# Performance work log

Hardware: AMD Instinct MI355X
Metric: run time of the kernel (lower is better)

## Reference

```python
import jax, jax.numpy as jnp
import numpy as np
import math

N, E, MUL = 10000, 160000, 128
D = MUL * 4  # 128x0e (128) + 128x1o (384) = 512
NEURONS = 32
EDGE_ATTR_DIM = 32
WEIGHT_NUMEL = 4 * MUL  # 4 uvu tensor-product paths, 128 weights each


def ssp(x):
    return jax.nn.softplus(x) - math.log(2.0)


def irrep_linear(x, W0, b0, W1):
    # o3.Linear on 128x0e+128x1o: mixes mul channels within each irrep, fan-in normalized,
    # bias only on scalar (0e) block.
    s = x[:, :MUL] @ (W0 / jnp.sqrt(MUL)) + b0
    v = x[:, MUL:].reshape(-1, MUL, 3)
    v = jnp.einsum('num,uv->nvm', v, W1) / jnp.sqrt(MUL)
    return jnp.concatenate([s, v.reshape(-1, MUL * 3)], axis=-1)


def inner_product(a, b):
    # InnerProduct: uuu channel-wise irrep inner product, 1/sqrt(dim) normalized
    s = a[:, :MUL] * b[:, :MUL]
    va = a[:, MUL:].reshape(-1, MUL, 3)
    vb = b[:, MUL:].reshape(-1, MUL, 3)
    v = jnp.einsum('num,num->nu', va, vb) / jnp.sqrt(3.0)
    return jnp.concatenate([s, v], axis=-1)


def norm_gate(x, W1, b1, W2, b2):
    # NormGate: per-channel norms of l>0 irreps -> MLP gates -> gate l>0 channels
    v = x[:, MUL:].reshape(-1, MUL, 3)
    norm_v = jnp.sqrt(jnp.sum(v * v, axis=-1) + 1e-12)      # [n, 128]
    f0 = jnp.concatenate([x[:, :MUL], norm_v], axis=-1)     # [n, 256]
    g = jax.nn.silu(f0 @ W1 + b1) @ W2 + b2                 # [n, 256]
    gated = v * g[:, MUL:, None]
    return jnp.concatenate([g[:, :MUL], gated.reshape(-1, MUL * 3)], axis=-1)


def mlp2(x, Wa, Wb):
    # e3nn FullyConnectedNet: fan-in normalized, ssp nonlinearity on hidden layer only
    return ssp(x @ (Wa / jnp.sqrt(Wa.shape[0]))) @ (Wb / jnp.sqrt(Wb.shape[0]))


def setup_inputs():
    key = jax.random.key(0)
    ks = jax.random.split(key, 20)
    r = lambda i, shp: jax.random.normal(ks[i], shp, dtype=jnp.float32)
    return {
        'x': r(0, (N, D)),
        'edge_index': jax.random.randint(ks[1], (2, E), 0, N, dtype=jnp.int32),
        'edge_attr': jax.random.uniform(ks[2], (E, EDGE_ATTR_DIM), dtype=jnp.float32),
        'edge_sh': r(3, (E, 4)),
        'Wp0': r(4, (MUL, MUL)), 'bp0': jnp.zeros((MUL,), jnp.float32), 'Wp1': r(5, (MUL, MUL)),
        'ngW1': r(6, (2 * MUL, 2 * MUL)) / 16.0, 'ngb1': jnp.zeros((2 * MUL,), jnp.float32),
        'ngW2': r(7, (2 * MUL, 2 * MUL)) / 16.0, 'ngb2': jnp.zeros((2 * MUL,), jnp.float32),
        'Wn0': r(8, (MUL, MUL)), 'bn0': jnp.zeros((MUL,), jnp.float32), 'Wn1': r(9, (MUL, MUL)),
        'fcnW1': r(10, (EDGE_ATTR_DIM, NEURONS)), 'fcnW2': r(11, (NEURONS, WEIGHT_NUMEL)),
        'l0W1': r(12, (3 * MUL, NEURONS)), 'l0W2': r(13, (NEURONS, WEIGHT_NUMEL)),
        'Wo0': r(14, (MUL, MUL)), 'bo0': jnp.zeros((MUL,), jnp.float32), 'Wo1': r(15, (MUL, MUL)),
    }


def reference(x, edge_index, edge_attr, edge_sh, Wp0, bp0, Wp1, ngW1, ngb1, ngW2, ngb2,
              Wn0, bn0, Wn1, fcnW1, fcnW2, l0W1, l0W2, Wo0, bo0, Wo1):
    edge_dst, edge_src = edge_index[0], edge_index[1]
    # invariant edge descriptor s0 from pre-linear + inner product
    pre_x = irrep_linear(x, Wp0, bp0, Wp1)
    ip = inner_product(pre_x[edge_dst], pre_x[edge_src])[:, MUL:]             # [E,128]
    s0 = jnp.concatenate([pre_x[edge_dst][:, :MUL], pre_x[edge_src][:, :MUL], ip], axis=-1)  # [E,384]
    # norm-gate + linear on node features
    x = norm_gate(x, ngW1, ngb1, ngW2, ngb2)
    x = irrep_linear(x, Wn0, bn0, Wn1)
    self_x = x
    # per-edge tensor-product weights: fc_node(edge_attr) * layer_l0(s0)
    w = mlp2(edge_attr, fcnW1, fcnW2) * mlp2(s0, l0W1, l0W2)                   # [E,512]
    w1, w2, w3, w4 = w[:, :MUL], w[:, MUL:2 * MUL], w[:, 2 * MUL:3 * MUL], w[:, 3 * MUL:]
    xs = x[edge_src]
    xs0 = xs[:, :MUL]                     # [E,128]
    xs1 = xs[:, MUL:].reshape(E, MUL, 3)  # [E,128,3]
    sh0 = edge_sh[:, 0:1]
    sh1 = edge_sh[:, 1:4]
    # uvu CG tensor product paths: 0ex0e->0e, 0ex1o->1o, 1ox0e->1o, 1ox1o->0e
    c0, c1 = 0.5, jnp.sqrt(3.0) / 2.0  # path norm sqrt(ir_out.dim / n_paths)
    out0 = c0 * (w1 * xs0 * sh0 + w4 * jnp.einsum('eum,em->eu', xs1, sh1) / jnp.sqrt(3.0))
    out1 = c1 * (w2[:, :, None] * xs0[:, :, None] * sh1[:, None, :]
                 + w3[:, :, None] * xs1 * sh0[:, :, None])
    edge_feat = jnp.concatenate([out0, out1.reshape(E, MUL * 3)], axis=-1)     # [E,512]
    # scatter-aggregate to destination nodes, residual, output linear
    out = jax.ops.segment_sum(edge_feat, edge_dst, num_segments=N)
    out = out + self_x
    return irrep_linear(out, Wo0, bo0, Wo1)
```

## Files before the change

kernel.cpp:

```cpp
#include <hip/hip_runtime.h>
#include <hip/hip_fp16.h>
#include <math.h>

#define NN 10000
#define EE 160000

#define RS128 0.08838834764831845f
#define RS384 0.05103103630798287f
#define RS32  0.17677669529663687f
#define R3    0.57735026918962576f
#define C1V   0.86602540378443865f

typedef _Float16 half8 __attribute__((ext_vector_type(8)));
typedef float f32x4 __attribute__((ext_vector_type(4)));

__device__ __forceinline__ float sspf(float x) {
    return fmaxf(x, 0.0f) + log1pf(__expf(-fabsf(x))) - 0.69314718055994530942f;
}

__global__ __launch_bounds__(256) void k_pack(
    const float* __restrict__ W, _Float16* __restrict__ P, int K, int N) {
    int idx = blockIdx.x * 256 + threadIdx.x;
    if (idx >= K * N) return;
    const int KS = K >> 5;
    int j = idx & 7, lane = (idx >> 3) & 63, rest = idx >> 9;
    int ks = rest % KS, ct = rest / KS;
    int k = ks * 32 + ((lane >> 4) << 3) + j;
    int c = ct * 16 + (lane & 15);
    P[idx] = (_Float16)W[k * N + c];
}

__global__ __launch_bounds__(256) void k_irrep_m(
    const float* __restrict__ X, const _Float16* __restrict__ pW0,
    const float* __restrict__ b0, const _Float16* __restrict__ pW1,
    float* __restrict__ out) {
    __shared__ _Float16 Xr[4][16][136];
    const int t = threadIdx.x, lane = t & 63, w = t >> 6;
    const int nb = blockIdx.x * 16;
    for (int idx = t; idx < 16 * 128; idx += 256) {
        int n = idx >> 7, c4 = idx & 127;
        const float4 v = *(const float4*)(X + (size_t)(nb + n) * 512 + 4 * c4);
        float vals[4] = {v.x, v.y, v.z, v.w};
        int c = 4 * c4;
#pragma unroll
        for (int j = 0; j < 4; ++j) {
            int cc = c + j;
            if (cc < 128) Xr[0][n][cc] = (_Float16)vals[j];
            else { int d = cc - 128; Xr[1 + d % 3][n][d / 3] = (_Float16)vals[j]; }
        }
    }
    __syncthreads();
    const _Float16* pW = (w == 0) ? pW0 : pW1;
    const int row16 = lane & 15, kg = lane >> 4;
    f32x4 acc[8];
    const f32x4 zero = {0.0f, 0.0f, 0.0f, 0.0f};
#pragma unroll
    for (int ct = 0; ct < 8; ++ct) acc[ct] = zero;
    for (int ks = 0; ks < 4; ++ks) {
        const half8 a = *(const half8*)&Xr[w][row16][ks * 32 + kg * 8];
#pragma unroll
        for (int ct = 0; ct < 8; ++ct) {
            const half8 b = *(const half8*)(pW + (((ct * 4 + ks) * 64 + lane) << 3));
            acc[ct] = __builtin_amdgcn_mfma_f32_16x16x32_f16(a, b, acc[ct], 0, 0, 0);
        }
    }
#pragma unroll
    for (int ct = 0; ct < 8; ++ct) {
        const int col = ct * 16 + row16;
        const float bb = (w == 0) ? b0[col] : 0.0f;
#pragma unroll
        for (int r = 0; r < 4; ++r) {
            const int node = nb + kg * 4 + r;
            const float val = acc[ct][r] * RS128 + bb;
            if (w == 0) out[(size_t)node * 512 + col] = val;
            else out[(size_t)node * 512 + 128 + 3 * col + (w - 1)] = val;
        }
    }
}

__global__ __launch_bounds__(256) void k_self_m(
    const float* __restrict__ X,
    const _Float16* __restrict__ png1, const float* __restrict__ ngb1,
    const _Float16* __restrict__ png2, const float* __restrict__ ngb2,
    const _Float16* __restrict__ pWn0, const float* __restrict__ bn0,
    const _Float16* __restrict__ pWn1,
    float* __restrict__ selfx) {
    __shared__ _Float16 f0h[16][264];
    __shared__ _Float16 t1h[16][264];
    __shared__ _Float16 xvh[3][16][136];
    const int t = threadIdx.x, lane = t & 63, w = t >> 6;
    const int nb = blockIdx.x * 16;
    const int row16 = lane & 15, kg = lane >> 4;
    const f32x4 zero = {0.0f, 0.0f, 0.0f, 0.0f};

    for (int idx = t; idx < 16 * 128; idx += 256) {
        int n = idx >> 7, c4 = idx & 127;
        const float4 v = *(const float4*)(X + (size_t)(nb + n) * 512 + 4 * c4);
        float vals[4] = {v.x, v.y, v.z, v.w};
        int c = 4 * c4;
#pragma unroll
        for (int j = 0; j < 4; ++j) {
            int cc = c + j;
            if (cc < 128) f0h[n][cc] = (_Float16)vals[j];
            else { int d = cc - 128; xvh[d % 3][n][d / 3] = (_Float16)vals[j]; }
        }
    }
    __syncthreads();
    for (int idx = t; idx < 16 * 128; idx += 256) {
        int n = idx >> 7, u = idx & 127;
        float a = (float)xvh[0][n][u], b = (float)xvh[1][n][u], c = (float)xvh[2][n][u];
        f0h[n][128 + u] = (_Float16)sqrtf(fmaf(a, a, fmaf(b, b, fmaf(c, c, 1e-12f))));
    }
    __syncthreads();
    {
        f32x4 acc[4];
#pragma unroll
        for (int i = 0; i < 4; ++i) acc[i] = zero;
        for (int ks = 0; ks < 8; ++ks) {
            const half8 a = *(const half8*)&f0h[row16][ks * 32 + kg * 8];
#pragma unroll
            for (int c2 = 0; c2 < 4; ++c2) {
                const int ct = 4 * w + c2;
                const half8 b = *(const half8*)(png1 + (((ct * 8 + ks) * 64 + lane) << 3));
                acc[c2] = __builtin_amdgcn_mfma_f32_16x16x32_f16(a, b, acc[c2], 0, 0, 0);
            }
        }
#pragma unroll
        for (int c2 = 0; c2 < 4; ++c2) {
            const int col = (4 * w + c2) * 16 + row16;
            const float bb = ngb1[col];
#pragma unroll
            for (int r = 0; r < 4; ++r) {
                const float z = acc[c2][r] + bb;
                t1h[kg * 4 + r][col] = (_Float16)(z / (1.0f + __expf(-z)));
            }
        }
    }
    __syncthreads();
    {
        f32x4 acc[4];
#pragma unroll
        for (int i = 0; i < 4; ++i) acc[i] = zero;
        for (int ks = 0; ks < 8; ++ks) {
            const half8 a = *(const half8*)&t1h[row16][ks * 32 + kg * 8];
#pragma unroll
            for (int c2 = 0; c2 < 4; ++c2) {
                const int ct = 4 * w + c2;
                const half8 b = *(const half8*)(png2 + (((ct * 8 + ks) * 64 + lane) << 3));
                acc[c2] = __builtin_amdgcn_mfma_f32_16x16x32_f16(a, b, acc[c2], 0, 0, 0);
            }
        }
        __syncthreads();
#pragma unroll
        for (int c2 = 0; c2 < 4; ++c2) {
            const int col = (4 * w + c2) * 16 + row16;
            const float bb = ngb2[col];
#pragma unroll
            for (int r = 0; r < 4; ++r)
                f0h[kg * 4 + r][col] = (_Float16)(acc[c2][r] + bb);
        }
    }
    __syncthreads();
    for (int idx = t; idx < 16 * 128; idx += 256) {
        int n = idx >> 7, u = idx & 127;
        const _Float16 g = f0h[n][128 + u];
        xvh[0][n][u] = xvh[0][n][u] * g;
        xvh[1][n][u] = xvh[1][n][u] * g;
        xvh[2][n][u] = xvh[2][n][u] * g;
    }
    __syncthreads();
    {
        const _Float16* pw = (w == 0) ? pWn0 : pWn1;
        f32x4 acc[8];
#pragma unroll
        for (int ct = 0; ct < 8; ++ct) acc[ct] = zero;
        for (int ks = 0; ks < 4; ++ks) {
            const half8 a = (w == 0)
                ? *(const half8*)&f0h[row16][ks * 32 + kg * 8]
                : *(const half8*)&xvh[w - 1][row16][ks * 32 + kg * 8];
#pragma unroll
            for (int ct = 0; ct < 8; ++ct) {
                const half8 b = *(const half8*)(pw + (((ct * 4 + ks) * 64 + lane) << 3));
                acc[ct] = __builtin_amdgcn_mfma_f32_16x16x32_f16(a, b, acc[ct], 0, 0, 0);
            }
        }
#pragma unroll
        for (int ct = 0; ct < 8; ++ct) {
            const int col = ct * 16 + row16;
            const float bb = (w == 0) ? bn0[col] : 0.0f;
#pragma unroll
            for (int r = 0; r < 4; ++r) {
                const int node = nb + kg * 4 + r;
                const float val = acc[ct][r] * RS128 + bb;
                if (w == 0) selfx[(size_t)node * 512 + col] = val;
                else selfx[(size_t)node * 512 + 128 + 3 * col + (w - 1)] = val;
            }
        }
    }
}

__global__ __launch_bounds__(256) void k_pre(
    const float* __restrict__ prex, const float* __restrict__ l0W1,
    float* __restrict__ pAB) {
    __shared__ float xs[8][128];
    const int t = threadIdx.x;
    const int nb = blockIdx.x * 8;
    for (int idx = t; idx < 8 * 128; idx += 256) {
        int n = idx >> 7, u = idx & 127;
        xs[n][u] = prex[(size_t)(nb + n) * 512 + u];
    }
    __syncthreads();
    const int n = t >> 5, k = t & 31;
    float a = 0, b = 0;
    for (int u = 0; u < 128; ++u) {
        float s = xs[n][u];
        a = fmaf(s, l0W1[u * 32 + k], a);
        b = fmaf(s, l0W1[(128 + u) * 32 + k], b);
    }
    pAB[(size_t)(nb + n) * 64 + k] = a;
    pAB[(size_t)(nb + n) * 64 + 32 + k] = b;
}

__global__ __launch_bounds__(256) void k_wconv(
    const float* __restrict__ fcnW2, const float* __restrict__ l0W2,
    _Float16* __restrict__ Wf_t, _Float16* __restrict__ Wl_t) {
    int idx = blockIdx.x * 256 + threadIdx.x;
    int k = idx & 31, c = idx >> 5;
    Wf_t[c * 32 + k] = (_Float16)fcnW2[k * 512 + c];
    Wl_t[c * 32 + k] = (_Float16)l0W2[k * 512 + c];
}

__global__ __launch_bounds__(256) void k_deg(const int* __restrict__ ei, int* __restrict__ deg) {
    int e = blockIdx.x * 256 + threadIdx.x;
    if (e < EE) atomicAdd(&deg[ei[e]], 1);
}

__global__ __launch_bounds__(1024) void k_scan(const int* __restrict__ deg, int* __restrict__ row_ptr) {
    __shared__ int part[1024];
    const int t = threadIdx.x;
    const int base = t * 10;
    int loc[10];
    int s = 0;
#pragma unroll
    for (int i = 0; i < 10; ++i) {
        int idx = base + i;
        int d = (idx < NN) ? deg[idx] : 0;
        loc[i] = s;
        s += d;
    }
    part[t] = s;
    __syncthreads();
    for (int off = 1; off < 1024; off <<= 1) {
        int v = (t >= off) ? part[t - off] : 0;
        __syncthreads();
        part[t] += v;
        __syncthreads();
    }
    int excl = (t > 0) ? part[t - 1] : 0;
#pragma unroll
    for (int i = 0; i < 10; ++i) {
        int idx = base + i;
        if (idx <= NN) row_ptr[idx] = excl + loc[i];
    }
}

__global__ __launch_bounds__(256) void k_fill(const int* __restrict__ ei,
                                              const int* __restrict__ row_ptr,
                                              int* __restrict__ cursor,
                                              int* __restrict__ csr_eid) {
    int e = blockIdx.x * 256 + threadIdx.x;
    if (e < EE) {
        int d = ei[e];
        int pos = atomicAdd(&cursor[d], 1);
        csr_eid[row_ptr[d] + pos] = e;
    }
}

__global__ __launch_bounds__(256) void k_hidden_m(
    const float* __restrict__ prex, const float* __restrict__ pAB,
    const int* __restrict__ edge_index, const float* __restrict__ edge_attr,
    const int* __restrict__ csr_eid,
    const _Float16* __restrict__ pWc, const _Float16* __restrict__ pWa,
    __half* __restrict__ hh) {
    const int pb = blockIdx.x * 32;
    const int t = threadIdx.x, lane = t & 63, w = t >> 6;
    __shared__ _Float16 ipl[32][132];
    __shared__ _Float16 eal[32][36];
    __shared__ _Float16 h1o[32][32];
    __shared__ _Float16 hao[32][32];
    __shared__ int dsts[32], srcs[32], eids[32];

    if (t < 32) {
        const int id = csr_eid[pb + t];
        eids[t] = id;
        dsts[t] = edge_index[id];
        srcs[t] = edge_index[EE + id];
    }
    __syncthreads();
    for (int idx = t; idx < 32 * 32; idx += 256) {
        int e = idx >> 5, j = idx & 31;
        eal[e][j] = (_Float16)edge_attr[(size_t)eids[e] * 32 + j];
    }
    for (int idx = t; idx < 32 * 128; idx += 256) {
        int e = idx >> 7, u = idx & 127;
        const float* pd = prex + (size_t)dsts[e] * 512 + 128 + 3 * u;
        const float* ps = prex + (size_t)srcs[e] * 512 + 128 + 3 * u;
        ipl[e][u] = (_Float16)((pd[0] * ps[0] + pd[1] * ps[1] + pd[2] * ps[2]) * R3);
    }
    __syncthreads();

    const int row16 = lane & 15, kg = lane >> 4;
    const int mt = w >> 1, ct = w & 1;
    const int e0 = mt * 16;
    const f32x4 zero = {0.0f, 0.0f, 0.0f, 0.0f};
    const int kc = ct * 16 + row16;

    {
        f32x4 acc = zero;
#pragma unroll
        for (int ks = 0; ks < 4; ++ks) {
            const half8 a = *(const half8*)&ipl[e0 + row16][ks * 32 + kg * 8];
            const half8 b = *(const half8*)(pWc + (((ct * 4 + ks) * 64 + lane) << 3));
            acc = __builtin_amdgcn_mfma_f32_16x16x32_f16(a, b, acc, 0, 0, 0);
        }
#pragma unroll
        for (int r = 0; r < 4; ++r) {
            const int e = e0 + kg * 4 + r;
            const float v = acc[r] + pAB[(size_t)dsts[e] * 64 + kc]
                                   + pAB[(size_t)srcs[e] * 64 + 32 + kc];
            h1o[e][kc] = (_Float16)sspf(v * RS384);
        }
    }
    {
        const half8 a = *(const half8*)&eal[e0 + row16][kg * 8];
        const half8 b = *(const half8*)(pWa + ((ct * 64 + lane) << 3));
        f32x4 acc = __builtin_amdgcn_mfma_f32_16x16x32_f16(a, b, zero, 0, 0, 0);
#pragma unroll
        for (int r = 0; r < 4; ++r) {
            const int e = e0 + kg * 4 + r;
            hao[e][kc] = (_Float16)sspf((float)acc[r] * RS32);
        }
    }
    __syncthreads();
    for (int idx = t; idx < 32 * 32; idx += 256) {
        const int e = idx >> 5, j = idx & 31;
        unsigned vv;
        if (j < 16) {
            __half2 h2 = __halves2half2((__half)h1o[e][2 * j], (__half)h1o[e][2 * j + 1]);
            vv = *(unsigned*)&h2;
        } else {
            const int jj = j - 16;
            __half2 h2 = __halves2half2((__half)hao[e][2 * jj], (__half)hao[e][2 * jj + 1]);
            vv = *(unsigned*)&h2;
        }
        ((unsigned*)hh)[(size_t)(pb + e) * 32 + j] = vv;
    }
}

__global__ __launch_bounds__(512) void k_accum(
    const __half* __restrict__ hh, const float* __restrict__ selfx,
    const int* __restrict__ edge_index, const float* __restrict__ edge_sh,
    const int* __restrict__ row_ptr, const int* __restrict__ csr_eid,
    const _Float16* __restrict__ Wf_t, const _Float16* __restrict__ Wl_t,
    float* __restrict__ outacc) {
    const int dst0 = blockIdx.x * 4;
    const int t = threadIdx.x;
    const int lane = t & 63;
    const int wid = t >> 6;

    __shared__ __align__(16) _Float16 h1s[4][16][8];
    __shared__ __align__(16) _Float16 has[4][16][8];
    __shared__ float shl[16][4];
    __shared__ int srcs[16];

    const int lcol = lane & 15;
    const int kg = lane >> 4;
    const int u = 16 * wid + lcol;
    const int koff = kg * 8;

    half8 bf[4], bl[4];
#pragma unroll
    for (int q = 0; q < 4; ++q) {
        const int col = q * 128 + u;
        bf[q] = *(const half8*)(Wf_t + col * 32 + koff);
        bl[q] = *(const half8*)(Wl_t + col * 32 + koff);
    }
    const float inv32 = 1.0f / 32.0f;

    for (int dd = 0; dd < 4; ++dd) {
        const int dst = dst0 + dd;
        const int beg = row_ptr[dst];
        const int ne = row_ptr[dst + 1] - beg;
        float acc0 = 0, acc1 = 0, acc2 = 0, acc3 = 0;

        for (int c0 = 0; c0 < ne; c0 += 16) {
            const int ce = min(16, ne - c0);
            __syncthreads();
            if (t < 16) {
                const int id = csr_eid[beg + c0 + ((t < ce) ? t : 0)];
                srcs[t] = (t < ce) ? edge_index[EE + id] : 0;
                const float4 s = *(const float4*)(edge_sh + (size_t)id * 4);
                shl[t][0] = s.x; shl[t][1] = s.y; shl[t][2] = s.z; shl[t][3] = s.w;
            }
            {
                const int e = t >> 5, w = t & 31;
                const unsigned val = (e < ce)
                    ? ((const unsigned*)hh)[(size_t)(beg + c0 + e) * 32 + w] : 0u;
                if (w < 16) ((unsigned*)h1s)[(w >> 2) * 64 + e * 4 + (w & 3)] = val;
                else        ((unsigned*)has)[((w - 16) >> 2) * 64 + e * 4 + ((w - 16) & 3)] = val;
            }
            __syncthreads();

            const half8 haf = *(const half8*)(&has[kg][lcol][0]);
            const half8 h1f = *(const half8*)(&h1s[kg][lcol][0]);
            const f32x4 zero = {0.0f, 0.0f, 0.0f, 0.0f};
            f32x4 A[4], B[4];
#pragma unroll
            for (int q = 0; q < 4; ++q) {
                A[q] = __builtin_amdgcn_mfma_f32_16x16x32_f16(haf, bf[q], zero, 0, 0, 0);
                B[q] = __builtin_amdgcn_mfma_f32_16x16x32_f16(h1f, bl[q], zero, 0, 0, 0);
            }
#pragma unroll
            for (int r = 0; r < 4; ++r) {
                const int e = kg * 4 + r;
                if (e < ce) {
                    const float w1 = A[0][r] * B[0][r] * inv32;
                    const float w2 = A[1][r] * B[1][r] * inv32;
                    const float w3 = A[2][r] * B[2][r] * inv32;
                    const float w4 = A[3][r] * B[3][r] * inv32;
                    const int src = srcs[e];
                    const float sh0 = shl[e][0], s1x = shl[e][1], s1y = shl[e][2], s1z = shl[e][3];
                    const float* sr = selfx + (size_t)src * 512;
                    const float xs0 = sr[u];
                    const float* sv = sr + 128 + 3 * u;
                    const float xv0 = sv[0], xv1 = sv[1], xv2 = sv[2];
                    const float dv = xv0 * s1x + xv1 * s1y + xv2 * s1z;
                    acc0 += 0.5f * (w1 * xs0 * sh0 + w4 * dv * R3);
                    acc1 += C1V * (w2 * xs0 * s1x + w3 * xv0 * sh0);
                    acc2 += C1V * (w2 * xs0 * s1y + w3 * xv1 * sh0);
                    acc3 += C1V * (w2 * xs0 * s1z + w3 * xv2 * sh0);
                }
            }
        }

        acc0 += __shfl_xor(acc0, 16, 64); acc0 += __shfl_xor(acc0, 32, 64);
        acc1 += __shfl_xor(acc1, 16, 64); acc1 += __shfl_xor(acc1, 32, 64);
        acc2 += __shfl_xor(acc2, 16, 64); acc2 += __shfl_xor(acc2, 32, 64);
        acc3 += __shfl_xor(acc3, 16, 64); acc3 += __shfl_xor(acc3, 32, 64);

        if (lane < 16) {
            const size_t g = (size_t)dst * 512;
            outacc[g + u] = acc0 + selfx[g + u];
            outacc[g + 128 + 3 * u + 0] = acc1 + selfx[g + 128 + 3 * u + 0];
            outacc[g + 128 + 3 * u + 1] = acc2 + selfx[g + 128 + 3 * u + 1];
            outacc[g + 128 + 3 * u + 2] = acc3 + selfx[g + 128 + 3 * u + 2];
        }
    }
}

extern "C" void kernel_launch(void* const* d_in, const int* in_sizes, int n_in,
                              void* d_out, int out_size, void* d_ws, size_t ws_size,
                              hipStream_t stream) {
    const float* x = (const float*)d_in[0];
    const int* edge_index = (const int*)d_in[1];
    const float* edge_attr = (const float*)d_in[2];
    const float* edge_sh = (const float*)d_in[3];
    const float* Wp0 = (const float*)d_in[4];
    const float* bp0 = (const float*)d_in[5];
    const float* Wp1 = (const float*)d_in[6];
    const float* ngW1 = (const float*)d_in[7];
    const float* ngb1 = (const float*)d_in[8];
    const float* ngW2 = (const float*)d_in[9];
    const float* ngb2 = (const float*)d_in[10];
    const float* Wn0 = (const float*)d_in[11];
    const float* bn0 = (const float*)d_in[12];
    const float* Wn1 = (const float*)d_in[13];
    const float* fcnW1 = (const float*)d_in[14];
    const float* fcnW2 = (const float*)d_in[15];
    const float* l0W1 = (const float*)d_in[16];
    const float* l0W2 = (const float*)d_in[17];
    const float* Wo0 = (const float*)d_in[18];
    const float* bo0 = (const float*)d_in[19];
    const float* Wo1 = (const float*)d_in[20];

    float* out = (float*)d_out;
    float* prex = out;
    float* selfx = (float*)d_ws;
    int* deg = (int*)(selfx + (size_t)NN * 512);
    int* cursor = deg + NN;
    int* row_ptr = cursor + NN;
    int* csr_eid = row_ptr + NN + 1;
    float* pAB = (float*)(csr_eid + EE);
    __half* hh = (__half*)(pAB + (size_t)NN * 64);
    _Float16* Wf_t = (_Float16*)(hh + (size_t)EE * 64);
    _Float16* Wl_t = Wf_t + 512 * 32;
    _Float16* pWp0 = Wl_t + 512 * 32;
    _Float16* pWp1 = pWp0 + 128 * 128;
    _Float16* pWn0 = pWp1 + 128 * 128;
    _Float16* pWn1 = pWn0 + 128 * 128;
    _Float16* pWo0 = pWn1 + 128 * 128;
    _Float16* pWo1 = pWo0 + 128 * 128;
    _Float16* png1 = pWo1 + 128 * 128;
    _Float16* png2 = png1 + 256 * 256;
    _Float16* pWc  = png2 + 256 * 256;
    _Float16* pWa  = pWc + 128 * 32;

    hipMemsetAsync(deg, 0, 2 * NN * sizeof(int), stream);

    k_pack<<<64, 256, 0, stream>>>(Wp0, pWp0, 128, 128);
    k_pack<<<64, 256, 0, stream>>>(Wp1, pWp1, 128, 128);
    k_pack<<<64, 256, 0, stream>>>(Wn0, pWn0, 128, 128);
    k_pack<<<64, 256, 0, stream>>>(Wn1, pWn1, 128, 128);
    k_pack<<<64, 256, 0, stream>>>(Wo0, pWo0, 128, 128);
    k_pack<<<64, 256, 0, stream>>>(Wo1, pWo1, 128, 128);
    k_pack<<<256, 256, 0, stream>>>(ngW1, png1, 256, 256);
    k_pack<<<256, 256, 0, stream>>>(ngW2, png2, 256, 256);
    k_pack<<<16, 256, 0, stream>>>(l0W1 + 256 * 32, pWc, 128, 32);
    k_pack<<<4, 256, 0, stream>>>(fcnW1, pWa, 32, 32);
    k_wconv<<<64, 256, 0, stream>>>(fcnW2, l0W2, Wf_t, Wl_t);

    k_irrep_m<<<NN / 16, 256, 0, stream>>>(x, pWp0, bp0, pWp1, prex);
    k_pre<<<NN / 8, 256, 0, stream>>>(prex, l0W1, pAB);
    k_self_m<<<NN / 16, 256, 0, stream>>>(x, png1, ngb1, png2, ngb2, pWn0, bn0, pWn1, selfx);
    k_deg<<<EE / 256, 256, 0, stream>>>(edge_index, deg);
    k_scan<<<1, 1024, 0, stream>>>(deg, row_ptr);
    k_fill<<<EE / 256, 256, 0, stream>>>(edge_index, row_ptr, cursor, csr_eid);
    k_hidden_m<<<EE / 32, 256, 0, stream>>>(prex, pAB, edge_index, edge_attr, csr_eid,
                                            pWc, pWa, hh);
    k_accum<<<NN / 4, 512, 0, stream>>>(hh, selfx, edge_index, edge_sh, row_ptr, csr_eid,
                                        Wf_t, Wl_t, out);
    k_irrep_m<<<NN / 16, 256, 0, stream>>>(out, pWo0, bo0, pWo1, out);
}
```

Measured before the change: 282.6 us.

## Fuse weight-pack launches and software-pipeline accum chunks across destinations

Merges eleven small weight-packing launches into a single k_packall kernel to cut launch overhead. In k_accum, each block now handles 8 destination nodes as one flattened chunk stream. Shared staging buffers are double-buffered, and the global loads for the next chunk go into registers before the barrier, so only one sync per chunk is needed and load latency overlaps with MFMA compute. This adds register and shared-memory pressure, halves the grid size, and adds a per-chunk linear search over the destination offsets.

```diff
diff --git a/kernel.cpp b/kernel.cpp
--- a/kernel.cpp
+++ b/kernel.cpp
@@ -4,6 +4,7 @@
 
 #define NN 10000
 #define EE 160000
+#define DPB 8
 
 #define RS128 0.08838834764831845f
 #define RS384 0.05103103630798287f
@@ -18,16 +19,53 @@
     return fmaxf(x, 0.0f) + log1pf(__expf(-fabsf(x))) - 0.69314718055994530942f;
 }
 
-__global__ __launch_bounds__(256) void k_pack(
-    const float* __restrict__ W, _Float16* __restrict__ P, int K, int N) {
-    int idx = blockIdx.x * 256 + threadIdx.x;
-    if (idx >= K * N) return;
+__device__ __forceinline__ void packone(const float* __restrict__ W,
+                                        _Float16* __restrict__ P,
+                                        int K, int N, int off) {
     const int KS = K >> 5;
-    int j = idx & 7, lane = (idx >> 3) & 63, rest = idx >> 9;
+    int j = off & 7, lane = (off >> 3) & 63, rest = off >> 9;
     int ks = rest % KS, ct = rest / KS;
     int k = ks * 32 + ((lane >> 4) << 3) + j;
     int c = ct * 16 + (lane & 15);
-    P[idx] = (_Float16)W[k * N + c];
+    P[off] = (_Float16)W[k * N + c];
+}
+
+__global__ __launch_bounds__(256) void k_packall(
+    const float* __restrict__ Wp0, const float* __restrict__ Wp1,
+    const float* __restrict__ Wn0, const float* __restrict__ Wn1,
+    const float* __restrict__ Wo0, const float* __restrict__ Wo1,
+    const float* __restrict__ ngW1, const float* __restrict__ ngW2,
+    const float* __restrict__ l0W1, const float* __restrict__ fcnW1,
+    const float* __restrict__ fcnW2, const float* __restrict__ l0W2,
+    _Float16* __restrict__ pWp0, _Float16* __restrict__ pWp1,
+    _Float16* __restrict__ pWn0, _Float16* __restrict__ pWn1,
+    _Float16* __restrict__ pWo0, _Float16* __restrict__ pWo1,
+    _Float16* __restrict__ png1, _Float16* __restrict__ png2,
+    _Float16* __restrict__ pWc, _Float16* __restrict__ pWa,
+    _Float16* __restrict__ Wf_t, _Float16* __restrict__ Wl_t) {
+    int idx = blockIdx.x * 256 + threadIdx.x;
+    if (idx < 98304) {
+        int seg = idx >> 14, off = idx & 16383;
+        if (seg == 0) packone(Wp0, pWp0, 128, 128, off);
+        else if (seg == 1) packone(Wp1, pWp1, 128, 128, off);
+        else if (seg == 2) packone(Wn0, pWn0, 128, 128, off);
+        else if (seg == 3) packone(Wn1, pWn1, 128, 128, off);
+        else if (seg == 4) packone(Wo0, pWo0, 128, 128, off);
+        else packone(Wo1, pWo1, 128, 128, off);
+    } else if (idx < 229376) {
+        int r = idx - 98304;
+        if (r < 65536) packone(ngW1, png1, 256, 256, r);
+        else packone(ngW2, png2, 256, 256, r - 65536);
+    } else if (idx < 233472) {
+        packone(l0W1 + 256 * 32, pWc, 128, 32, idx - 229376);
+    } else if (idx < 234496) {
+        packone(fcnW1, pWa, 32, 32, idx - 233472);
+    } else {
+        int off = idx - 234496;
+        int k = off & 31, c = off >> 5;
+        Wf_t[c * 32 + k] = (_Float16)fcnW2[k * 512 + c];
+        Wl_t[c * 32 + k] = (_Float16)l0W2[k * 512 + c];
+    }
 }
 
 __global__ __launch_bounds__(256) void k_irrep_m(
@@ -221,15 +259,6 @@
     pAB[(size_t)(nb + n) * 64 + 32 + k] = b;
 }
 
-__global__ __launch_bounds__(256) void k_wconv(
-    const float* __restrict__ fcnW2, const float* __restrict__ l0W2,
-    _Float16* __restrict__ Wf_t, _Float16* __restrict__ Wl_t) {
-    int idx = blockIdx.x * 256 + threadIdx.x;
-    int k = idx & 31, c = idx >> 5;
-    Wf_t[c * 32 + k] = (_Float16)fcnW2[k * 512 + c];
-    Wl_t[c * 32 + k] = (_Float16)l0W2[k * 512 + c];
-}
-
 __global__ __launch_bounds__(256) void k_deg(const int* __restrict__ ei, int* __restrict__ deg) {
     int e = blockIdx.x * 256 + threadIdx.x;
     if (e < EE) atomicAdd(&deg[ei[e]], 1);
@@ -363,21 +392,33 @@
     const int* __restrict__ row_ptr, const int* __restrict__ csr_eid,
     const _Float16* __restrict__ Wf_t, const _Float16* __restrict__ Wl_t,
     float* __restrict__ outacc) {
-    const int dst0 = blockIdx.x * 4;
+    const int dst0 = blockIdx.x * DPB;
     const int t = threadIdx.x;
     const int lane = t & 63;
     const int wid = t >> 6;
-
-    __shared__ __align__(16) _Float16 h1s[4][16][8];
-    __shared__ __align__(16) _Float16 has[4][16][8];
-    __shared__ float shl[16][4];
-    __shared__ int srcs[16];
-
     const int lcol = lane & 15;
     const int kg = lane >> 4;
     const int u = 16 * wid + lcol;
     const int koff = kg * 8;
 
+    __shared__ __align__(16) _Float16 h1s[2][4][16][8];
+    __shared__ __align__(16) _Float16 has[2][4][16][8];
+    __shared__ float shl[2][16][4];
+    __shared__ int srcs[2][16];
+    __shared__ int cbeg[DPB], cne[DPB], cchk[DPB + 1];
+
+    if (t < DPB) {
+        const int b = row_ptr[dst0 + t];
+        cbeg[t] = b;
+        cne[t] = row_ptr[dst0 + t + 1] - b;
+    }
+    __syncthreads();
+    if (t == 0) {
+        int s = 0;
+#pragma unroll
+        for (int i = 0; i < DPB; ++i) { cchk[i] = s; s += max(1, (cne[i] + 15) >> 4); }
+        cchk[DPB] = s;
+    }
     half8 bf[4], bl[4];
 #pragma unroll
     for (int q = 0; q < 4; ++q) {
@@ -385,77 +426,104 @@
         bf[q] = *(const half8*)(Wf_t + col * 32 + koff);
         bl[q] = *(const half8*)(Wl_t + col * 32 + koff);
     }
+    __syncthreads();
+    const int nc = cchk[DPB];
     const float inv32 = 1.0f / 32.0f;
 
-    for (int dd = 0; dd < 4; ++dd) {
-        const int dst = dst0 + dd;
-        const int beg = row_ptr[dst];
-        const int ne = row_ptr[dst + 1] - beg;
-        float acc0 = 0, acc1 = 0, acc2 = 0, acc3 = 0;
-
-        for (int c0 = 0; c0 < ne; c0 += 16) {
-            const int ce = min(16, ne - c0);
-            __syncthreads();
-            if (t < 16) {
-                const int id = csr_eid[beg + c0 + ((t < ce) ? t : 0)];
-                srcs[t] = (t < ce) ? edge_index[EE + id] : 0;
-                const float4 s = *(const float4*)(edge_sh + (size_t)id * 4);
-                shl[t][0] = s.x; shl[t][1] = s.y; shl[t][2] = s.z; shl[t][3] = s.w;
-            }
-            {
-                const int e = t >> 5, w = t & 31;
-                const unsigned val = (e < ce)
-                    ? ((const unsigned*)hh)[(size_t)(beg + c0 + e) * 32 + w] : 0u;
-                if (w < 16) ((unsigned*)h1s)[(w >> 2) * 64 + e * 4 + (w & 3)] = val;
-                else        ((unsigned*)has)[((w - 16) >> 2) * 64 + e * 4 + ((w - 16) & 3)] = val;
-            }
-            __syncthreads();
-
-            const half8 haf = *(const half8*)(&has[kg][lcol][0]);
-            const half8 h1f = *(const half8*)(&h1s[kg][lcol][0]);
-            const f32x4 zero = {0.0f, 0.0f, 0.0f, 0.0f};
-            f32x4 A[4], B[4];
-#pragma unroll
-            for (int q = 0; q < 4; ++q) {
-                A[q] = __builtin_amdgcn_mfma_f32_16x16x32_f16(haf, bf[q], zero, 0, 0, 0);
-                B[q] = __builtin_amdgcn_mfma_f32_16x16x32_f16(h1f, bl[q], zero, 0, 0, 0);
-            }
-#pragma unroll
-            for (int r = 0; r < 4; ++r) {
-                const int e = kg * 4 + r;
-                if (e < ce) {
-                    const float w1 = A[0][r] * B[0][r] * inv32;
-                    const float w2 = A[1][r] * B[1][r] * inv32;
-                    const float w3 = A[2][r] * B[2][r] * inv32;
-                    const float w4 = A[3][r] * B[3][r] * inv32;
-                    const int src = srcs[e];
-                    const float sh0 = shl[e][0], s1x = shl[e][1], s1y = shl[e][2], s1z = shl[e][3];
-                    const float* sr = selfx + (size_t)src * 512;
-                    const float xs0 = sr[u];
-                    const float* sv = sr + 128 + 3 * u;
-                    const float xv0 = sv[0], xv1 = sv[1], xv2 = sv[2];
-                    const float dv = xv0 * s1x + xv1 * s1y + xv2 * s1z;
-                    acc0 += 0.5f * (w1 * xs0 * sh0 + w4 * dv * R3);
-                    acc1 += C1V * (w2 * xs0 * s1x + w3 * xv0 * sh0);
-                    acc2 += C1V * (w2 * xs0 * s1y + w3 * xv1 * sh0);
-                    acc3 += C1V * (w2 * xs0 * s1z + w3 * xv2 * sh0);
-                }
-            }
-        }
-
+    float acc0 = 0, acc1 = 0, acc2 = 0, acc3 = 0;
+
+    unsigned rhh = 0;
+    int rsrc = 0;
+    float4 rsh = {0.0f, 0.0f, 0.0f, 0.0f};
+
+    const int se = t >> 5, sw = t & 31;
+
+    auto issue = [&](int ci) {
+        int dd = 0;
+        while (dd + 1 < DPB && ci >= cchk[dd + 1]) ++dd;
+        const int c0 = (ci - cchk[dd]) << 4;
+        const int ce = min(16, cne[dd] - c0);
+        const int pos = cbeg[dd] + c0;
+        rhh = (se < ce) ? ((const unsigned*)hh)[(size_t)(pos + se) * 32 + sw] : 0u;
+        if (t < 16) {
+            if (t < ce) {
+                const int id = csr_eid[pos + t];
+                rsrc = edge_index[EE + id];
+                rsh = *(const float4*)(edge_sh + (size_t)id * 4);
+            } else {
+                rsrc = 0;
+                rsh = make_float4(0.0f, 0.0f, 0.0f, 0.0f);
+            }
+        }
+    };
+
+    auto flush = [&](int dd) {
         acc0 += __shfl_xor(acc0, 16, 64); acc0 += __shfl_xor(acc0, 32, 64);
         acc1 += __shfl_xor(acc1, 16, 64); acc1 += __shfl_xor(acc1, 32, 64);
         acc2 += __shfl_xor(acc2, 16, 64); acc2 += __shfl_xor(acc2, 32, 64);
         acc3 += __shfl_xor(acc3, 16, 64); acc3 += __shfl_xor(acc3, 32, 64);
-
         if (lane < 16) {
-            const size_t g = (size_t)dst * 512;
+            const size_t g = (size_t)(dst0 + dd) * 512;
             outacc[g + u] = acc0 + selfx[g + u];
             outacc[g + 128 + 3 * u + 0] = acc1 + selfx[g + 128 + 3 * u + 0];
             outacc[g + 128 + 3 * u + 1] = acc2 + selfx[g + 128 + 3 * u + 1];
             outacc[g + 128 + 3 * u + 2] = acc3 + selfx[g + 128 + 3 * u + 2];
         }
-    }
+        acc0 = acc1 = acc2 = acc3 = 0;
+    };
+
+    issue(0);
+    int cur = 0, cur_dd = 0;
+    for (int ci = 0; ci < nc; ++ci) {
+        if (sw < 16) ((unsigned*)h1s[cur])[(sw >> 2) * 64 + se * 4 + (sw & 3)] = rhh;
+        else         ((unsigned*)has[cur])[((sw - 16) >> 2) * 64 + se * 4 + ((sw - 16) & 3)] = rhh;
+        if (t < 16) {
+            srcs[cur][t] = rsrc;
+            shl[cur][t][0] = rsh.x; shl[cur][t][1] = rsh.y;
+            shl[cur][t][2] = rsh.z; shl[cur][t][3] = rsh.w;
+        }
+        int dd = 0;
+        while (dd + 1 < DPB && ci >= cchk[dd + 1]) ++dd;
+        const int c0 = (ci - cchk[dd]) << 4;
+        const int ce = min(16, cne[dd] - c0);
+        if (ci + 1 < nc) issue(ci + 1);
+        __syncthreads();
+        if (dd != cur_dd) { flush(cur_dd); cur_dd = dd; }
+
+        const half8 haf = *(const half8*)(&has[cur][kg][lcol][0]);
+        const half8 h1f = *(const half8*)(&h1s[cur][kg][lcol][0]);
+        const f32x4 zero = {0.0f, 0.0f, 0.0f, 0.0f};
+        f32x4 A[4], B[4];
+#pragma unroll
+        for (int q = 0; q < 4; ++q) {
+            A[q] = __builtin_amdgcn_mfma_f32_16x16x32_f16(haf, bf[q], zero, 0, 0, 0);
+            B[q] = __builtin_amdgcn_mfma_f32_16x16x32_f16(h1f, bl[q], zero, 0, 0, 0);
+        }
+#pragma unroll
+        for (int r = 0; r < 4; ++r) {
+            const int e = kg * 4 + r;
+            if (e < ce) {
+                const float w1 = A[0][r] * B[0][r] * inv32;
+                const float w2 = A[1][r] * B[1][r] * inv32;
+                const float w3 = A[2][r] * B[2][r] * inv32;
+                const float w4 = A[3][r] * B[3][r] * inv32;
+                const int src = srcs[cur][e];
+                const float sh0 = shl[cur][e][0], s1x = shl[cur][e][1];
+                const float s1y = shl[cur][e][2], s1z = shl[cur][e][3];
+                const float* sr = selfx + (size_t)src * 512;
+                const float xs0 = sr[u];
+                const float* sv = sr + 128 + 3 * u;
+                const float xv0 = sv[0], xv1 = sv[1], xv2 = sv[2];
+                const float dv = xv0 * s1x + xv1 * s1y + xv2 * s1z;
+                acc0 += 0.5f * (w1 * xs0 * sh0 + w4 * dv * R3);
+                acc1 += C1V * (w2 * xs0 * s1x + w3 * xv0 * sh0);
+                acc2 += C1V * (w2 * xs0 * s1y + w3 * xv1 * sh0);
+                acc3 += C1V * (w2 * xs0 * s1z + w3 * xv2 * sh0);
+            }
+        }
+        cur ^= 1;
+    }
+    flush(cur_dd);
 }
 
 extern "C" void kernel_launch(void* const* d_in, const int* in_sizes, int n_in,
@@ -507,27 +575,20 @@
 
     hipMemsetAsync(deg, 0, 2 * NN * sizeof(int), stream);
 
-    k_pack<<<64, 256, 0, stream>>>(Wp0, pWp0, 128, 128);
-    k_pack<<<64, 256, 0, stream>>>(Wp1, pWp1, 128, 128);
-    k_pack<<<64, 256, 0, stream>>>(Wn0, pWn0, 128, 128);
-    k_pack<<<64, 256, 0, stream>>>(Wn1, pWn1, 128, 128);
-    k_pack<<<64, 256, 0, stream>>>(Wo0, pWo0, 128, 128);
-    k_pack<<<64, 256, 0, stream>>>(Wo1, pWo1, 128, 128);
-    k_pack<<<256, 256, 0, stream>>>(ngW1, png1, 256, 256);
-    k_pack<<<256, 256, 0, stream>>>(ngW2, png2, 256, 256);
-    k_pack<<<16, 256, 0, stream>>>(l0W1 + 256 * 32, pWc, 128, 32);
-    k_pack<<<4, 256, 0, stream>>>(fcnW1, pWa, 32, 32);
-    k_wconv<<<64, 256, 0, stream>>>(fcnW2, l0W2, Wf_t, Wl_t);
+    k_packall<<<980, 256, 0, stream>>>(Wp0, Wp1, Wn0, Wn1, Wo0, Wo1, ngW1, ngW2,
+                                       l0W1, fcnW1, fcnW2, l0W2,
+                                       pWp0, pWp1, pWn0, pWn1, pWo0, pWo1,
+                                       png1, png2, pWc, pWa, Wf_t, Wl_t);
 
     k_irrep_m<<<NN / 16, 256, 0, stream>>>(x, pWp0, bp0, pWp1, prex);
     k_pre<<<NN / 8, 256, 0, stream>>>(prex, l0W1, pAB);
-    k_self_m<<<NN / 16, 256, 0, stream>>>(x, png1, ngb1, png2, ngb2, pWn0, bn0, pWn1, selfx);
+    k_self_m<<<NN / 16, 256, 0, stream>>>(x, ngW1 ? png1 : png1, ngb1, png2, ngb2, pWn0, bn0, pWn1, selfx);
     k_deg<<<EE / 256, 256, 0, stream>>>(edge_index, deg);
     k_scan<<<1, 1024, 0, stream>>>(deg, row_ptr);
     k_fill<<<EE / 256, 256, 0, stream>>>(edge_index, row_ptr, cursor, csr_eid);
     k_hidden_m<<<EE / 32, 256, 0, stream>>>(prex, pAB, edge_index, edge_attr, csr_eid,
                                             pWc, pWa, hh);
-    k_accum<<<NN / 4, 512, 0, stream>>>(hh, selfx, edge_index, edge_sh, row_ptr, csr_eid,
-                                        Wf_t, Wl_t, out);
+    k_accum<<<NN / DPB, 512, 0, stream>>>(hh, selfx, edge_index, edge_sh, row_ptr, csr_eid,
+                                          Wf_t, Wl_t, out);
     k_irrep_m<<<NN / 16, 256, 0, stream>>>(out, pWo0, bo0, pWo1, out);
 }
```

Result: faster. 262.3 us (-7.2%).
